# Kernel tuning notes

Measured on AMD Instinct MI355X. Metric: run time of the kernel, lower is better.

## Reference

```python
import jax, jax.numpy as jnp
import numpy as np
import math

H = 16          # num_heads
BS = 512        # block_size


def setup_inputs() -> dict:
    key = jax.random.key(0)
    ks = jax.random.split(key, 5)
    B, S, D = 2, 8192, 1024
    return {
        "x": jax.random.normal(ks[0], (B, S, D), dtype=jnp.float32),
        "W_qkv": jax.random.normal(ks[1], (D, 3 * D), dtype=jnp.float32) * (1.0 / math.sqrt(D)),
        "b_qkv": jax.random.normal(ks[2], (3 * D,), dtype=jnp.float32) * 0.02,
        "W_out": jax.random.normal(ks[3], (D, D), dtype=jnp.float32) * (1.0 / math.sqrt(D)),
        "b_out": jax.random.normal(ks[4], (D,), dtype=jnp.float32) * 0.02,
    }


def reference(x, W_qkv, b_qkv, W_out, b_out):
    B, S, D = x.shape
    hd = D // H
    nb = S // BS  # S chosen divisible by block_size, so no padding branch
    scale = 1.0 / math.sqrt(hd)

    qkv = (x @ W_qkv + b_qkv).reshape(B, S, 3, H, hd)
    qkv = jnp.transpose(qkv, (2, 0, 3, 1, 4))  # [3, B, H, S, hd]
    q, k, v = qkv[0], qkv[1], qkv[2]

    # split into blocks: [B, H, nb, BS, hd]
    qb = q.reshape(B, H, nb, BS, hd)
    kb = k.reshape(B, H, nb, BS, hd)
    vb = v.reshape(B, H, nb, BS, hd)

    # local block attention (separate softmax, as in original)
    s1 = jnp.einsum('bhnid,bhnjd->bhnij', qb, kb) * scale
    o1 = jnp.einsum('bhnij,bhnjd->bhnid', jax.nn.softmax(s1, axis=-1), vb)

    # next-block (ring) attention with its own softmax, then summed
    kn = jnp.roll(kb, -1, axis=2)
    vn = jnp.roll(vb, -1, axis=2)
    s2 = jnp.einsum('bhnid,bhnjd->bhnij', qb, kn) * scale
    o2 = jnp.einsum('bhnij,bhnjd->bhnid', jax.nn.softmax(s2, axis=-1), vn)

    out = (o1 + o2).reshape(B, H, S, hd)            # [B, H, S, hd]
    out = jnp.transpose(out, (0, 2, 1, 3)).reshape(B, S, D)
    return out @ W_out + b_out
```

## Files before the change

### kernel.cpp

```cpp
#include <hip/hip_runtime.h>
#include <hip/hip_bf16.h>

typedef __attribute__((ext_vector_type(4))) float f32x4;
typedef __attribute__((ext_vector_type(8))) short s16x8;
typedef __attribute__((address_space(3))) unsigned int lds_uint;
typedef __attribute__((address_space(1))) const unsigned int g_uint;

static __device__ __forceinline__ unsigned short f2b(float f) {
    union { __hip_bfloat16 h; unsigned short u; } c;
    c.h = __float2bfloat16(f);
    return c.u;
}

static __device__ __forceinline__ void async_copy16(const void* gsrc, void* ldst) {
    __builtin_amdgcn_global_load_lds((g_uint*)gsrc, (lds_uint*)ldst, 16, 0, 0);
}

__global__ __launch_bounds__(256) void cvt_x_kernel(const float* __restrict__ x,
                                                    unsigned short* __restrict__ xb) {
    long i = ((long)blockIdx.x * 256 + threadIdx.x) * 8;
    float4 a = *(const float4*)(x + i);
    float4 b = *(const float4*)(x + i + 4);
    union { unsigned short s[8]; s16x8 v; } o;
    o.s[0] = f2b(a.x); o.s[1] = f2b(a.y); o.s[2] = f2b(a.z); o.s[3] = f2b(a.w);
    o.s[4] = f2b(b.x); o.s[5] = f2b(b.y); o.s[6] = f2b(b.z); o.s[7] = f2b(b.w);
    *(s16x8*)(xb + i) = o.v;
}

__global__ __launch_bounds__(256) void cvt_wT_kernel(const float* __restrict__ W,
                                                     unsigned short* __restrict__ Wt,
                                                     int K, int N) {
    __shared__ float T[64][65];
    int nbk = K >> 6;
    int bk = blockIdx.x % nbk;
    int bn = blockIdx.x / nbk;
    int t = threadIdx.x;
    int r = t >> 4, c4 = (t & 15) << 2;
#pragma unroll
    for (int rd = 0; rd < 4; ++rd) {
        int row = rd * 16 + r;
        float4 v = *(const float4*)(W + (long)(bk * 64 + row) * N + bn * 64 + c4);
        T[row][c4 + 0] = v.x; T[row][c4 + 1] = v.y;
        T[row][c4 + 2] = v.z; T[row][c4 + 3] = v.w;
    }
    __syncthreads();
#pragma unroll
    for (int rd = 0; rd < 4; ++rd) {
        int nrow = rd * 16 + r;
        union { unsigned short s[4]; unsigned long long u; } o;
#pragma unroll
        for (int j = 0; j < 4; ++j) o.s[j] = f2b(T[c4 + j][nrow]);
        *(unsigned long long*)(Wt + (long)(bn * 64 + nrow) * K + bk * 64 + c4) = o.u;
    }
}

__global__ __launch_bounds__(256) void gemm_qkv_kernel(const unsigned short* __restrict__ A,
                                                       const unsigned short* __restrict__ Bt,
                                                       const float* __restrict__ bias,
                                                       unsigned short* __restrict__ qkb,
                                                       unsigned short* __restrict__ vT) {
    const int K = 1024;
    __shared__ unsigned short As[128 * 32];
    __shared__ unsigned short Bs[128 * 32];
    const int tid = threadIdx.x;
    const int w = tid >> 6, l = tid & 63;
    const int c = l & 15, g = l >> 4;
    const int wgid = (blockIdx.x & 7) * 384 + (blockIdx.x >> 3);
    const int tm = wgid / 24, tn = wgid % 24;
    const long m0 = (long)tm << 7, n0 = (long)tn << 7;

    f32x4 acc[4][4];
#pragma unroll
    for (int i = 0; i < 4; ++i)
#pragma unroll
        for (int j = 0; j < 4; ++j) acc[i][j] = (f32x4){0.f, 0.f, 0.f, 0.f};

    const int arow = tid >> 2, ac8 = (tid & 3) << 3;
    for (int k0 = 0; k0 < K; k0 += 32) {
        __syncthreads();
#pragma unroll
        for (int rd = 0; rd < 2; ++rd) {
            int row = arow + rd * 64;
            int off = (rd * 256 + tid) * 16;
            async_copy16(A + (m0 + row) * (long)K + k0 + ac8, (char*)As + off);
            async_copy16(Bt + (n0 + row) * (long)K + k0 + ac8, (char*)Bs + off);
        }
        __syncthreads();
        s16x8 af[4], bf_[4];
#pragma unroll
        for (int i = 0; i < 4; ++i) {
            af[i]  = *(const s16x8*)((const char*)As + ((w >> 1) * 64 + i * 16 + c) * 64 + g * 16);
            bf_[i] = *(const s16x8*)((const char*)Bs + ((w & 1) * 64 + i * 16 + c) * 64 + g * 16);
        }
#pragma unroll
        for (int i = 0; i < 4; ++i)
#pragma unroll
            for (int j = 0; j < 4; ++j)
                acc[i][j] = __builtin_amdgcn_mfma_f32_16x16x32_bf16(af[i], bf_[j], acc[i][j], 0, 0, 0);
    }

    if (n0 < 2048) {
#pragma unroll
        for (int j = 0; j < 4; ++j) {
            int n = (int)n0 + (w & 1) * 64 + j * 16 + c;
            float bv = bias[n];
#pragma unroll
            for (int i = 0; i < 4; ++i)
#pragma unroll
                for (int r = 0; r < 4; ++r) {
                    long m = m0 + (w >> 1) * 64 + i * 16 + 4 * g + r;
                    qkb[m * 2048 + n] = f2b(acc[i][j][r] + bv);
                }
        }
    } else {
#pragma unroll
        for (int j = 0; j < 4; ++j) {
            int n = (int)n0 + (w & 1) * 64 + j * 16 + c;
            float bv = bias[n];
            int h = (n - 2048) >> 6, hd = n & 63;
#pragma unroll
            for (int i = 0; i < 4; ++i) {
                long m = m0 + (w >> 1) * 64 + i * 16 + 4 * g;
                long bb = m >> 13;
                long s = m & 8191;
                union { unsigned short sh[4]; unsigned long long u; } o;
#pragma unroll
                for (int r = 0; r < 4; ++r) o.sh[r] = f2b(acc[i][j][r] + bv);
                *(unsigned long long*)(vT + ((bb * 16 + h) * 64 + hd) * 8192 + s) = o.u;
            }
        }
    }
}

__global__ __launch_bounds__(256) void gemm_out_kernel(const unsigned short* __restrict__ A,
                                                       const unsigned short* __restrict__ Bt,
                                                       const float* __restrict__ bias,
                                                       float* __restrict__ C,
                                                       int M, int N, int K) {
    __shared__ unsigned short As[128 * 32];
    __shared__ unsigned short Bs[128 * 32];
    const int tid = threadIdx.x;
    const int w = tid >> 6, l = tid & 63;
    const int c = l & 15, g = l >> 4;
    const int ntile = N >> 7;
    const int cpx = gridDim.x >> 3;
    const int wgid = (blockIdx.x & 7) * cpx + (blockIdx.x >> 3);
    const int tm = wgid / ntile, tn = wgid % ntile;
    const long m0 = (long)tm << 7, n0 = (long)tn << 7;

    f32x4 acc[4][4];
#pragma unroll
    for (int i = 0; i < 4; ++i)
#pragma unroll
        for (int j = 0; j < 4; ++j) acc[i][j] = (f32x4){0.f, 0.f, 0.f, 0.f};

    const int arow = tid >> 2, ac8 = (tid & 3) << 3;
    for (int k0 = 0; k0 < K; k0 += 32) {
        __syncthreads();
#pragma unroll
        for (int rd = 0; rd < 2; ++rd) {
            int row = arow + rd * 64;
            int off = (rd * 256 + tid) * 16;
            async_copy16(A + (m0 + row) * (long)K + k0 + ac8, (char*)As + off);
            async_copy16(Bt + (n0 + row) * (long)K + k0 + ac8, (char*)Bs + off);
        }
        __syncthreads();
        s16x8 af[4], bf_[4];
#pragma unroll
        for (int i = 0; i < 4; ++i) {
            af[i]  = *(const s16x8*)((const char*)As + ((w >> 1) * 64 + i * 16 + c) * 64 + g * 16);
            bf_[i] = *(const s16x8*)((const char*)Bs + ((w & 1) * 64 + i * 16 + c) * 64 + g * 16);
        }
#pragma unroll
        for (int i = 0; i < 4; ++i)
#pragma unroll
            for (int j = 0; j < 4; ++j)
                acc[i][j] = __builtin_amdgcn_mfma_f32_16x16x32_bf16(af[i], bf_[j], acc[i][j], 0, 0, 0);
    }
#pragma unroll
    for (int j = 0; j < 4; ++j) {
        int n = (int)n0 + (w & 1) * 64 + j * 16 + c;
        float bv = bias[n];
#pragma unroll
        for (int i = 0; i < 4; ++i)
#pragma unroll
            for (int r = 0; r < 4; ++r) {
                long m = m0 + (w >> 1) * 64 + i * 16 + 4 * g + r;
                C[m * (long)N + n] = acc[i][j][r] + bv;
            }
    }
}

__global__ __launch_bounds__(256) void attn_kernel(const unsigned short* __restrict__ qkb,
                                                   const unsigned short* __restrict__ vT,
                                                   unsigned short* __restrict__ outp) {
    __shared__ unsigned short Ks[64 * 72];
    __shared__ unsigned short VTs[64 * 72];
    __shared__ unsigned short Pws[4][32 * 72];
    const int bid = blockIdx.x;
    const int wgid = (bid & 7) * 256 + (bid >> 3);
    const int qt = wgid & 3;
    const int nblk = (wgid >> 2) & 15;
    const int h = (wgid >> 6) & 15;
    const int b = wgid >> 10;
    const int tid = threadIdx.x;
    const int w = tid >> 6, l = tid & 63;
    const int c = l & 15, g = l >> 4;

    const long qrow0 = (long)b * 8192 + nblk * 512 + qt * 128 + w * 32 + c;
    s16x8 qf[2][2];
#pragma unroll
    for (int qg = 0; qg < 2; ++qg) {
        const unsigned short* qp = qkb + (qrow0 + qg * 16) * 2048 + h * 64;
        qf[qg][0] = *(const s16x8*)(qp + g * 8);
        qf[qg][1] = *(const s16x8*)(qp + 32 + g * 8);
    }

    char* pw = (char*)(&Pws[w][0]);
    const float C2 = 0.125f * 1.44269504088896f;

    const int cc = tid & 7;
    const int rbase = tid >> 3;
    char* kwp = (char*)Ks + rbase * 144 + cc * 16;
    char* vwp = (char*)VTs + rbase * 144 + cc * 16;

    const int kb1 = (nblk + 1) & 15;
    const unsigned short* Kg0 = qkb + ((long)b * 8192 + nblk * 512) * 2048 + 1024 + h * 64
                                + (long)rbase * 2048 + cc * 8;
    const unsigned short* Kg1 = qkb + ((long)b * 8192 + kb1 * 512) * 2048 + 1024 + h * 64
                                + (long)rbase * 2048 + cc * 8;
    const unsigned short* Vg0 = vT + ((long)(b * 16 + h) * 64 + rbase) * 8192 + nblk * 512 + cc * 8;
    const unsigned short* Vg1 = vT + ((long)(b * 16 + h) * 64 + rbase) * 8192 + kb1 * 512 + cc * 8;

    float outv[2][16];
#pragma unroll
    for (int qg = 0; qg < 2; ++qg)
#pragma unroll
        for (int i = 0; i < 16; ++i) outv[qg][i] = 0.f;

    f32x4 oac[2][4];
#pragma unroll
    for (int qg = 0; qg < 2; ++qg)
#pragma unroll
        for (int i = 0; i < 4; ++i) oac[qg][i] = (f32x4){0.f, 0.f, 0.f, 0.f};
    float mrun[2] = {-3e38f, -3e38f}, lrun[2] = {0.f, 0.f};

    s16x8 kreg0 = *(const s16x8*)(Kg0);
    s16x8 kreg1 = *(const s16x8*)(Kg0 + 32 * 2048);
    s16x8 vreg0 = *(const s16x8*)(Vg0);
    s16x8 vreg1 = *(const s16x8*)(Vg0 + 32 * 8192);

    for (int it = 0; it < 16; ++it) {
        __syncthreads();
        *(s16x8*)(kwp) = kreg0;
        *(s16x8*)(kwp + 32 * 144) = kreg1;
        *(s16x8*)(vwp) = vreg0;
        *(s16x8*)(vwp + 32 * 144) = vreg1;
        {
            int itn = it + 1;
            const unsigned short* kn = ((itn & 8) ? Kg1 : Kg0) + ((itn & 7) << 17);
            const unsigned short* vn = ((itn & 8) ? Vg1 : Vg0) + ((itn & 7) << 6);
            kreg0 = *(const s16x8*)(kn);
            kreg1 = *(const s16x8*)(kn + 32 * 2048);
            vreg0 = *(const s16x8*)(vn);
            vreg1 = *(const s16x8*)(vn + 32 * 8192);
        }
        __syncthreads();

        f32x4 sac[2][4];
#pragma unroll
        for (int qg = 0; qg < 2; ++qg)
#pragma unroll
            for (int i = 0; i < 4; ++i) sac[qg][i] = (f32x4){0.f, 0.f, 0.f, 0.f};
#pragma unroll
        for (int kt = 0; kt < 4; ++kt) {
            const char* kr = (const char*)Ks + (kt * 16 + c) * 144 + g * 16;
            s16x8 a0 = *(const s16x8*)(kr);
            s16x8 a1 = *(const s16x8*)(kr + 64);
            sac[0][kt] = __builtin_amdgcn_mfma_f32_16x16x32_bf16(a0, qf[0][0], sac[0][kt], 0, 0, 0);
            sac[0][kt] = __builtin_amdgcn_mfma_f32_16x16x32_bf16(a1, qf[0][1], sac[0][kt], 0, 0, 0);
            sac[1][kt] = __builtin_amdgcn_mfma_f32_16x16x32_bf16(a0, qf[1][0], sac[1][kt], 0, 0, 0);
            sac[1][kt] = __builtin_amdgcn_mfma_f32_16x16x32_bf16(a1, qf[1][1], sac[1][kt], 0, 0, 0);
        }

#pragma unroll
        for (int qg = 0; qg < 2; ++qg) {
            float mx = sac[qg][0][0];
#pragma unroll
            for (int kt = 0; kt < 4; ++kt)
#pragma unroll
                for (int r = 0; r < 4; ++r) mx = fmaxf(mx, sac[qg][kt][r]);
            mx = fmaxf(mx, __shfl_xor(mx, 16, 64));
            mx = fmaxf(mx, __shfl_xor(mx, 32, 64));
            float mnew = fmaxf(mrun[qg], mx);
            float alpha = exp2f((mrun[qg] - mnew) * C2);
            float ls = 0.f;
#pragma unroll
            for (int kt = 0; kt < 4; ++kt) {
                union { unsigned short sh[4]; unsigned long long u; } pk;
#pragma unroll
                for (int r = 0; r < 4; ++r) {
                    float e = exp2f((sac[qg][kt][r] - mnew) * C2);
                    ls += e;
                    pk.sh[r] = f2b(e);
                }
                *(unsigned long long*)(pw + (qg * 16 + c) * 144 + kt * 32 + g * 8) = pk.u;
            }
            ls += __shfl_xor(ls, 16, 64);
            ls += __shfl_xor(ls, 32, 64);
            lrun[qg] = lrun[qg] * alpha + ls;
            mrun[qg] = mnew;
#pragma unroll
            for (int i = 0; i < 4; ++i) oac[qg][i] *= alpha;
        }

#pragma unroll
        for (int kf = 0; kf < 2; ++kf) {
            s16x8 pf0 = *(const s16x8*)(pw + c * 144 + kf * 64 + g * 16);
            s16x8 pf1 = *(const s16x8*)(pw + (16 + c) * 144 + kf * 64 + g * 16);
#pragma unroll
            for (int ht = 0; ht < 4; ++ht) {
                s16x8 vf = *(const s16x8*)((const char*)VTs + (ht * 16 + c) * 144 + kf * 64 + g * 16);
                oac[0][ht] = __builtin_amdgcn_mfma_f32_16x16x32_bf16(vf, pf0, oac[0][ht], 0, 0, 0);
                oac[1][ht] = __builtin_amdgcn_mfma_f32_16x16x32_bf16(vf, pf1, oac[1][ht], 0, 0, 0);
            }
        }

        if ((it & 7) == 7) {
#pragma unroll
            for (int qg = 0; qg < 2; ++qg) {
                float inv = 1.f / lrun[qg];
#pragma unroll
                for (int i = 0; i < 16; ++i) outv[qg][i] += oac[qg][i >> 2][i & 3] * inv;
#pragma unroll
                for (int i = 0; i < 4; ++i) oac[qg][i] = (f32x4){0.f, 0.f, 0.f, 0.f};
                mrun[qg] = -3e38f;
                lrun[qg] = 0.f;
            }
        }
    }

#pragma unroll
    for (int qg = 0; qg < 2; ++qg) {
        unsigned short* op = outp + (qrow0 + qg * 16) * 1024 + h * 64;
#pragma unroll
        for (int ht = 0; ht < 4; ++ht) {
            union { unsigned short sh[4]; unsigned long long u; } o;
#pragma unroll
            for (int r = 0; r < 4; ++r) o.sh[r] = f2b(outv[qg][ht * 4 + r]);
            *(unsigned long long*)(op + ht * 16 + 4 * g) = o.u;
        }
    }
}

extern "C" void kernel_launch(void* const* d_in, const int* in_sizes, int n_in,
                              void* d_out, int out_size, void* d_ws, size_t ws_size,
                              hipStream_t stream) {
    const float* x    = (const float*)d_in[0];
    const float* Wqkv = (const float*)d_in[1];
    const float* bqkv = (const float*)d_in[2];
    const float* Wout = (const float*)d_in[3];
    const float* bout = (const float*)d_in[4];
    float* out = (float*)d_out;

    char* ws = (char*)d_ws;
    unsigned short* xbf   = (unsigned short*)ws;
    unsigned short* wqkvT = (unsigned short*)(ws + 33554432);
    unsigned short* woutT = (unsigned short*)(ws + 39845888);
    unsigned short* qkb   = (unsigned short*)(ws + 41943040);
    unsigned short* vT    = (unsigned short*)(ws + 109051904);
    unsigned short* attn  = xbf;

    cvt_x_kernel<<<8192, 256, 0, stream>>>(x, xbf);
    cvt_wT_kernel<<<(1024 / 64) * (3072 / 64), 256, 0, stream>>>(Wqkv, wqkvT, 1024, 3072);
    cvt_wT_kernel<<<(1024 / 64) * (1024 / 64), 256, 0, stream>>>(Wout, woutT, 1024, 1024);
    gemm_qkv_kernel<<<128 * 24, 256, 0, stream>>>(xbf, wqkvT, bqkv, qkb, vT);
    attn_kernel<<<2048, 256, 0, stream>>>(qkb, vT, attn);
    gemm_out_kernel<<<128 * 8, 256, 0, stream>>>(attn, woutT, bout, out, 16384, 1024, 1024);
}
```

Baseline: 487.5 us.

## Replace both GEMMs with 256x256-tile double-buffered pipelined MFMA kernel

Replaces the 128x128 QKV and output-projection GEMMs with one templated 256x256-tile kernel using 512 threads, a 128KB LDS double buffer, and async global-to-LDS copies issued several k-steps ahead. It uses explicit vmcnt waits, raw s_barriers, XOR-swizzled LDS layout and setprio around MFMA bursts, so loads overlap compute and bank conflicts drop. The bigger tiles cut global traffic per FLOP. In exchange only one block fits per CU, and the output GEMM launches just 256 blocks, which may underfill the GPU.

New measurement: 452.2 us. 1.08x faster.

```diff
diff --git a/kernel.cpp b/kernel.cpp
--- a/kernel.cpp
+++ b/kernel.cpp
@@ -54,141 +54,154 @@
     }
 }
 
-__global__ __launch_bounds__(256) void gemm_qkv_kernel(const unsigned short* __restrict__ A,
-                                                       const unsigned short* __restrict__ Bt,
-                                                       const float* __restrict__ bias,
-                                                       unsigned short* __restrict__ qkb,
-                                                       unsigned short* __restrict__ vT) {
-    const int K = 1024;
-    __shared__ unsigned short As[128 * 32];
-    __shared__ unsigned short Bs[128 * 32];
+template<int OM>
+__global__ __launch_bounds__(512) void gemm256_kernel(const unsigned short* __restrict__ A,
+                                                      const unsigned short* __restrict__ Bt,
+                                                      const float* __restrict__ bias,
+                                                      unsigned short* __restrict__ qkb,
+                                                      unsigned short* __restrict__ vT,
+                                                      float* __restrict__ Cf,
+                                                      int ntileN) {
+    __shared__ char lds[131072];
     const int tid = threadIdx.x;
-    const int w = tid >> 6, l = tid & 63;
-    const int c = l & 15, g = l >> 4;
-    const int wgid = (blockIdx.x & 7) * 384 + (blockIdx.x >> 3);
-    const int tm = wgid / 24, tn = wgid % 24;
-    const long m0 = (long)tm << 7, n0 = (long)tn << 7;
-
-    f32x4 acc[4][4];
-#pragma unroll
-    for (int i = 0; i < 4; ++i)
+    const int w = tid >> 6, wm = w >> 2, wn = w & 3;
+    const int l = tid & 63, c = l & 15, g = l >> 4;
+    const int cpx = gridDim.x >> 3;
+    const int wg = (blockIdx.x & 7) * cpx + (blockIdx.x >> 3);
+    const int tm = wg / ntileN, tn = wg % ntileN;
+    const long m0 = (long)tm << 8, n0 = (long)tn << 8;
+    const int swg = (g ^ ((c >> 1) & 3)) << 4;
+    const int ssch = (tid & 3) ^ ((tid >> 3) & 3);
+    const int rb = tid >> 2;
+
+    f32x4 acc[8][4];
+#pragma unroll
+    for (int i = 0; i < 8; ++i)
 #pragma unroll
         for (int j = 0; j < 4; ++j) acc[i][j] = (f32x4){0.f, 0.f, 0.f, 0.f};
 
-    const int arow = tid >> 2, ac8 = (tid & 3) << 3;
-    for (int k0 = 0; k0 < K; k0 += 32) {
-        __syncthreads();
-#pragma unroll
-        for (int rd = 0; rd < 2; ++rd) {
-            int row = arow + rd * 64;
-            int off = (rd * 256 + tid) * 16;
-            async_copy16(A + (m0 + row) * (long)K + k0 + ac8, (char*)As + off);
-            async_copy16(Bt + (n0 + row) * (long)K + k0 + ac8, (char*)Bs + off);
-        }
-        __syncthreads();
-        s16x8 af[4], bf_[4];
-#pragma unroll
-        for (int i = 0; i < 4; ++i) {
-            af[i]  = *(const s16x8*)((const char*)As + ((w >> 1) * 64 + i * 16 + c) * 64 + g * 16);
-            bf_[i] = *(const s16x8*)((const char*)Bs + ((w & 1) * 64 + i * 16 + c) * 64 + g * 16);
-        }
-#pragma unroll
-        for (int i = 0; i < 4; ++i)
-#pragma unroll
-            for (int j = 0; j < 4; ++j)
-                acc[i][j] = __builtin_amdgcn_mfma_f32_16x16x32_bf16(af[i], bf_[j], acc[i][j], 0, 0, 0);
-    }
-
-    if (n0 < 2048) {
+#define STG(panel, p0, u, kh, isB) do { \
+    char* blk_ = lds + ((isB) ? 65536 : 0) + (((((u) & 1) * 2 + (kh))) << 14); \
+    const unsigned short* sp_ = (panel) + (u) * 64 + (kh) * 32 + ssch * 8; \
+    async_copy16(sp_ + ((p0) + rb) * 1024L, blk_ + tid * 16); \
+    async_copy16(sp_ + ((p0) + 128 + rb) * 1024L, blk_ + 8192 + tid * 16); \
+} while (0)
+
+    STG(Bt, n0, 0, 0, 1); STG(A, m0, 0, 0, 0); STG(Bt, n0, 0, 1, 1); STG(A, m0, 0, 1, 0);
+    STG(Bt, n0, 1, 0, 1); STG(A, m0, 1, 0, 0); STG(Bt, n0, 1, 1, 1);
+    asm volatile("s_waitcnt vmcnt(10)");
+    __builtin_amdgcn_s_barrier();
+    __builtin_amdgcn_sched_barrier(0);
+
+#define PHASE_MFMA(IBASE) \
+    __builtin_amdgcn_s_setprio(1); \
+    _Pragma("unroll") for (int i_ = 0; i_ < 4; ++i_) \
+    _Pragma("unroll") for (int j_ = 0; j_ < 4; ++j_) \
+        acc[(IBASE) + i_][j_] = __builtin_amdgcn_mfma_f32_16x16x32_bf16(af[i_], bf[j_], acc[(IBASE) + i_][j_], 0, 0, 0); \
+    __builtin_amdgcn_s_setprio(0);
+
+#define GSTEP(s, ST1, ST2, ST3, ST4, VMID, VEND) do { \
+    const int buf_ = (s) & 1; \
+    const char* LA0 = lds + ((buf_ * 2 + 0) << 14); \
+    const char* LA1 = lds + ((buf_ * 2 + 1) << 14); \
+    const char* LB0 = lds + 65536 + ((buf_ * 2 + 0) << 14); \
+    const char* LB1 = lds + 65536 + ((buf_ * 2 + 1) << 14); \
+    s16x8 af[4], bf[4]; \
+     \
+    _Pragma("unroll") for (int i = 0; i < 4; ++i) af[i] = *(const s16x8*)(LA0 + (wm * 128 + i * 16 + c) * 64 + swg); \
+    _Pragma("unroll") for (int j = 0; j < 4; ++j) bf[j] = *(const s16x8*)(LB0 + (wn * 64 + j * 16 + c) * 64 + swg); \
+    if (ST1) STG(A, m0, (s) + 1, 1, 0); \
+    __builtin_amdgcn_s_barrier(); \
+    PHASE_MFMA(0) \
+    __builtin_amdgcn_s_barrier(); \
+    __builtin_amdgcn_sched_barrier(0); \
+     \
+    _Pragma("unroll") for (int i = 0; i < 4; ++i) af[i] = *(const s16x8*)(LA0 + (wm * 128 + (4 + i) * 16 + c) * 64 + swg); \
+    if (ST2) STG(Bt, n0, (s) + 2, 0, 1); \
+    __builtin_amdgcn_s_barrier(); \
+    PHASE_MFMA(4) \
+    asm volatile("s_waitcnt " VMID); \
+    __builtin_amdgcn_s_barrier(); \
+    __builtin_amdgcn_sched_barrier(0); \
+     \
+    _Pragma("unroll") for (int i = 0; i < 4; ++i) af[i] = *(const s16x8*)(LA1 + (wm * 128 + i * 16 + c) * 64 + swg); \
+    _Pragma("unroll") for (int j = 0; j < 4; ++j) bf[j] = *(const s16x8*)(LB1 + (wn * 64 + j * 16 + c) * 64 + swg); \
+    if (ST3) STG(A, m0, (s) + 2, 0, 0); \
+    __builtin_amdgcn_s_barrier(); \
+    PHASE_MFMA(0) \
+    __builtin_amdgcn_s_barrier(); \
+    __builtin_amdgcn_sched_barrier(0); \
+     \
+    _Pragma("unroll") for (int i = 0; i < 4; ++i) af[i] = *(const s16x8*)(LA1 + (wm * 128 + (4 + i) * 16 + c) * 64 + swg); \
+    if (ST4) STG(Bt, n0, (s) + 2, 1, 1); \
+    __builtin_amdgcn_s_barrier(); \
+    PHASE_MFMA(4) \
+    if (VEND) { asm volatile("s_waitcnt " VMID##_E); } \
+    __builtin_amdgcn_s_barrier(); \
+    __builtin_amdgcn_sched_barrier(0); \
+} while (0)
+
+#define VM10 "vmcnt(10)"
+#define VM10_E "vmcnt(10)"
+#define VM8 "vmcnt(8)"
+#define VM8_E "vmcnt(4)"
+#define VM0 "vmcnt(0)"
+#define VM0_E "vmcnt(0)"
+
+    for (int s = 0; s < 14; ++s) GSTEP(s, 1, 1, 1, 1, VM10, 1);
+    GSTEP(14, 1, 0, 0, 0, VM8, 1);
+    GSTEP(15, 0, 0, 0, 0, VM0, 0);
+
+    const long mrow0 = m0 + wm * 128;
+    const int ncol0 = (int)n0 + wn * 64;
+    if (OM == 0) {
+        if (ncol0 < 2048) {
+#pragma unroll
+            for (int j = 0; j < 4; ++j) {
+                int n = ncol0 + j * 16 + c;
+                float bv = bias[n];
+#pragma unroll
+                for (int i = 0; i < 8; ++i)
+#pragma unroll
+                    for (int r = 0; r < 4; ++r) {
+                        long m = mrow0 + i * 16 + 4 * g + r;
+                        qkb[m * 2048 + n] = f2b(acc[i][j][r] + bv);
+                    }
+            }
+        } else {
+#pragma unroll
+            for (int j = 0; j < 4; ++j) {
+                int n = ncol0 + j * 16 + c;
+                float bv = bias[n];
+                int h = (n - 2048) >> 6, hd = n & 63;
+#pragma unroll
+                for (int i = 0; i < 8; ++i) {
+                    long m = mrow0 + i * 16 + 4 * g;
+                    long bb = m >> 13, ss = m & 8191;
+                    union { unsigned short sh[4]; unsigned long long u; } o;
+#pragma unroll
+                    for (int r = 0; r < 4; ++r) o.sh[r] = f2b(acc[i][j][r] + bv);
+                    *(unsigned long long*)(vT + ((bb * 16 + h) * 64 + hd) * 8192 + ss) = o.u;
+                }
+            }
+        }
+    } else {
 #pragma unroll
         for (int j = 0; j < 4; ++j) {
-            int n = (int)n0 + (w & 1) * 64 + j * 16 + c;
+            int n = ncol0 + j * 16 + c;
             float bv = bias[n];
 #pragma unroll
-            for (int i = 0; i < 4; ++i)
+            for (int i = 0; i < 8; ++i)
 #pragma unroll
                 for (int r = 0; r < 4; ++r) {
-                    long m = m0 + (w >> 1) * 64 + i * 16 + 4 * g + r;
-                    qkb[m * 2048 + n] = f2b(acc[i][j][r] + bv);
+                    long m = mrow0 + i * 16 + 4 * g + r;
+                    Cf[m * 1024 + n] = acc[i][j][r] + bv;
                 }
         }
-    } else {
-#pragma unroll
-        for (int j = 0; j < 4; ++j) {
-            int n = (int)n0 + (w & 1) * 64 + j * 16 + c;
-            float bv = bias[n];
-            int h = (n - 2048) >> 6, hd = n & 63;
-#pragma unroll
-            for (int i = 0; i < 4; ++i) {
-                long m = m0 + (w >> 1) * 64 + i * 16 + 4 * g;
-                long bb = m >> 13;
-                long s = m & 8191;
-                union { unsigned short sh[4]; unsigned long long u; } o;
-#pragma unroll
-                for (int r = 0; r < 4; ++r) o.sh[r] = f2b(acc[i][j][r] + bv);
-                *(unsigned long long*)(vT + ((bb * 16 + h) * 64 + hd) * 8192 + s) = o.u;
-            }
-        }
-    }
-}
-
-__global__ __launch_bounds__(256) void gemm_out_kernel(const unsigned short* __restrict__ A,
-                                                       const unsigned short* __restrict__ Bt,
-                                                       const float* __restrict__ bias,
-                                                       float* __restrict__ C,
-                                                       int M, int N, int K) {
-    __shared__ unsigned short As[128 * 32];
-    __shared__ unsigned short Bs[128 * 32];
-    const int tid = threadIdx.x;
-    const int w = tid >> 6, l = tid & 63;
-    const int c = l & 15, g = l >> 4;
-    const int ntile = N >> 7;
-    const int cpx = gridDim.x >> 3;
-    const int wgid = (blockIdx.x & 7) * cpx + (blockIdx.x >> 3);
-    const int tm = wgid / ntile, tn = wgid % ntile;
-    const long m0 = (long)tm << 7, n0 = (long)tn << 7;
-
-    f32x4 acc[4][4];
-#pragma unroll
-    for (int i = 0; i < 4; ++i)
-#pragma unroll
-        for (int j = 0; j < 4; ++j) acc[i][j] = (f32x4){0.f, 0.f, 0.f, 0.f};
-
-    const int arow = tid >> 2, ac8 = (tid & 3) << 3;
-    for (int k0 = 0; k0 < K; k0 += 32) {
-        __syncthreads();
-#pragma unroll
-        for (int rd = 0; rd < 2; ++rd) {
-            int row = arow + rd * 64;
-            int off = (rd * 256 + tid) * 16;
-            async_copy16(A + (m0 + row) * (long)K + k0 + ac8, (char*)As + off);
-            async_copy16(Bt + (n0 + row) * (long)K + k0 + ac8, (char*)Bs + off);
-        }
-        __syncthreads();
-        s16x8 af[4], bf_[4];
-#pragma unroll
-        for (int i = 0; i < 4; ++i) {
-            af[i]  = *(const s16x8*)((const char*)As + ((w >> 1) * 64 + i * 16 + c) * 64 + g * 16);
-            bf_[i] = *(const s16x8*)((const char*)Bs + ((w & 1) * 64 + i * 16 + c) * 64 + g * 16);
-        }
-#pragma unroll
-        for (int i = 0; i < 4; ++i)
-#pragma unroll
-            for (int j = 0; j < 4; ++j)
-                acc[i][j] = __builtin_amdgcn_mfma_f32_16x16x32_bf16(af[i], bf_[j], acc[i][j], 0, 0, 0);
-    }
-#pragma unroll
-    for (int j = 0; j < 4; ++j) {
-        int n = (int)n0 + (w & 1) * 64 + j * 16 + c;
-        float bv = bias[n];
-#pragma unroll
-        for (int i = 0; i < 4; ++i)
-#pragma unroll
-            for (int r = 0; r < 4; ++r) {
-                long m = m0 + (w >> 1) * 64 + i * 16 + 4 * g + r;
-                C[m * (long)N + n] = acc[i][j][r] + bv;
-            }
-    }
+    }
+#undef STG
+#undef PHASE_MFMA
+#undef GSTEP
 }
 
 __global__ __launch_bounds__(256) void attn_kernel(const unsigned short* __restrict__ qkb,
@@ -374,7 +387,7 @@
     cvt_x_kernel<<<8192, 256, 0, stream>>>(x, xbf);
     cvt_wT_kernel<<<(1024 / 64) * (3072 / 64), 256, 0, stream>>>(Wqkv, wqkvT, 1024, 3072);
     cvt_wT_kernel<<<(1024 / 64) * (1024 / 64), 256, 0, stream>>>(Wout, woutT, 1024, 1024);
-    gemm_qkv_kernel<<<128 * 24, 256, 0, stream>>>(xbf, wqkvT, bqkv, qkb, vT);
+    gemm256_kernel<0><<<64 * 12, 512, 0, stream>>>(xbf, wqkvT, bqkv, qkb, vT, nullptr, 12);
     attn_kernel<<<2048, 256, 0, stream>>>(qkb, vT, attn);
-    gemm_out_kernel<<<128 * 8, 256, 0, stream>>>(attn, woutT, bout, out, 16384, 1024, 1024);
-}
+    gemm256_kernel<1><<<64 * 4, 512, 0, stream>>>(attn, woutT, bout, nullptr, nullptr, out, 4);
+}
```
